# Optimization experiments

Hardware: AMD Instinct MI355X
Metric: run time of the kernel (lower is better)

## Reference

```python
import jax, jax.numpy as jnp
import numpy as np

GROUPS = 8
EPS = 1e-5
V, CIN, COUT, K, TDIM, B = 49152, 128, 256, 8, 256, 1
E = V * 9


def group_norm(x, gamma, beta):
    # x: [B, V, C]; torch GroupNorm semantics: normalize over (pixels, channels-in-group)
    b, v, c = x.shape
    xg = x.reshape(b, v, GROUPS, c // GROUPS)
    mu = xg.mean(axis=(1, 3), keepdims=True)
    var = xg.var(axis=(1, 3), keepdims=True)
    xg = (xg - mu) * jax.lax.rsqrt(var + EPS)
    return xg.reshape(b, v, c) * gamma + beta


def cheb_conv(x, row, col, vals, w):
    # x: [B, V, C]; w: [K, C, F]; Chebyshev recurrence on sparse Laplacian
    b, v, c = x.shape
    k = w.shape[0]
    xt = x.transpose(1, 0, 2).reshape(v, b * c)  # [V, B*C]

    def spmv(z):  # sparse L @ z via scatter-add
        return jnp.zeros_like(z).at[row].add(vals[:, None] * z[col])

    terms = [xt]
    if k > 1:
        terms.append(spmv(xt))
    for _ in range(k - 2):
        terms.append(2.0 * spmv(terms[-1]) - terms[-2])
    t = jnp.stack(terms).reshape(k, v, b, c)  # [K, V, B, C]
    return jnp.einsum('kvbc,kcf->bvf', t, w)  # [B, V, F]


def setup_inputs() -> dict:
    key = jax.random.key(0)
    ks = jax.random.split(key, 12)
    return {
        'x': jax.random.normal(ks[0], (B, V, CIN), jnp.float32),
        'time_emb': jax.random.normal(ks[1], (B, TDIM), jnp.float32),
        'row': jax.random.randint(ks[2], (E,), 0, V),
        'col': jax.random.randint(ks[3], (E,), 0, V),
        'vals': jax.random.normal(ks[4], (E,), jnp.float32) * 0.1,
        'w_res': jax.random.normal(ks[5], (K, CIN, COUT), jnp.float32) * 0.05,
        'w1': jax.random.normal(ks[6], (K, CIN, COUT), jnp.float32) * 0.05,
        'w2': jax.random.normal(ks[7], (K, COUT, COUT), jnp.float32) * 0.05,
        'g1': jnp.ones((CIN,), jnp.float32),
        'b1': jnp.zeros((CIN,), jnp.float32),
        'g2': jnp.ones((COUT,), jnp.float32),
        'b2': jnp.zeros((COUT,), jnp.float32),
        'wt': jax.random.normal(ks[8], (TDIM, COUT), jnp.float32) * 0.05,
        'bt': jnp.zeros((COUT,), jnp.float32),
    }


def reference(x, time_emb, row, col, vals, w_res, w1, w2, g1, b1, g2, b2, wt, bt):
    # conv_res (in_channels != out_channels), pooling = identity
    res = cheb_conv(x, row, col, vals, w_res)
    # block1: conv(silu(group_norm(x)))
    h = cheb_conv(jax.nn.silu(group_norm(x, g1, b1)), row, col, vals, w1)
    # time embedding: SiLU -> Linear -> broadcast over pixels
    h = h + (jax.nn.silu(time_emb) @ wt + bt)[:, None, :]
    # block2
    h = cheb_conv(jax.nn.silu(group_norm(h, g2, b2)), row, col, vals, w2)
    return h + res
```

## Files before the change

kernel.cpp:

```cpp
#include <hip/hip_runtime.h>
#include <cstddef>

#define V_N 49152
#define E_N 442368
#define E_PAD 589824
#define GEPS 1e-5f
#define CO 256
#define TD 256

typedef _Float16 h16;
typedef _Float16 h8v __attribute__((ext_vector_type(8)));
typedef _Float16 h4v __attribute__((ext_vector_type(4)));
typedef float f4v __attribute__((ext_vector_type(4)));

__device__ __forceinline__ void gload_lds16(const void* g, void* l) {
    __builtin_amdgcn_global_load_lds(
        (const __attribute__((address_space(1))) unsigned int*)g,
        (__attribute__((address_space(3))) unsigned int*)l, 16, 0, 0);
}

__global__ void count_edges(const int* __restrict__ row, int* __restrict__ cnt) {
    int e = blockIdx.x * blockDim.x + threadIdx.x;
    if (e < E_N) atomicAdd(&cnt[row[e]], 1);
}

__global__ void scan_rowptr(int* __restrict__ cnt, int* __restrict__ rowptr) {
    __shared__ int part[1024];
    const int CHUNK = V_N / 1024;
    int t = threadIdx.x;
    int base = t * CHUNK;
    int s = 0;
    for (int i = 0; i < CHUNK; ++i) s += (cnt[base + i] + 3) & ~3;
    part[t] = s;
    __syncthreads();
    for (int off = 1; off < 1024; off <<= 1) {
        int v = part[t];
        int add = (t >= off) ? part[t - off] : 0;
        __syncthreads();
        part[t] = v + add;
        __syncthreads();
    }
    int run = (t == 0) ? 0 : part[t - 1];
    for (int i = 0; i < CHUNK; ++i) {
        int c = cnt[base + i];
        rowptr[base + i] = run;
        cnt[base + i] = run;
        run += (c + 3) & ~3;
    }
    if (t == 1023) rowptr[V_N] = run;
}

__global__ void fill_csr(const int* __restrict__ row, const int* __restrict__ col,
                         const float* __restrict__ vals, int* __restrict__ cursor,
                         int2* __restrict__ ep) {
    int e = blockIdx.x * blockDim.x + threadIdx.x;
    if (e < E_N) {
        int r = row[e];
        int slot = atomicAdd(&cursor[r], 1);
        ep[slot] = make_int2(col[e], __float_as_int(vals[e]));
    }
}

__global__ void wprep_frag(const float* __restrict__ w, h16* __restrict__ wf) {
    int ks = blockIdx.x, nt = blockIdx.y, lane = threadIdx.x;
    int fr = lane & 15, fq = lane >> 4;
    int f = nt * 16 + fr;
    h8v o;
#pragma unroll
    for (int jj = 0; jj < 8; ++jj) {
        int kc = ks * 32 + fq * 8 + jj;
        o[jj] = (h16)w[(size_t)kc * CO + f];
    }
    *(h8v*)&wf[(((size_t)ks * 16 + nt) * 64 + lane) * 8] = o;
}

template <int C>
__global__ void gn_stats2(const float* __restrict__ x, const float* __restrict__ tvec,
                          float* __restrict__ part) {
    __shared__ float ls[8], lss[8];
    int t = threadIdx.x;
    if (t < 8) { ls[t] = 0.f; lss[t] = 0.f; }
    __syncthreads();
    const int total4 = V_N * (C / 4);
    const int cmask = (C / 4) - 1;
    const int stride = gridDim.x * blockDim.x;
    int i0 = blockIdx.x * blockDim.x + t;
    const int c4 = i0 & cmask;
    float t0 = 0.f, t1 = 0.f, t2 = 0.f, t3 = 0.f;
    if (tvec) {
        t0 = tvec[c4 * 4 + 0]; t1 = tvec[c4 * 4 + 1];
        t2 = tvec[c4 * 4 + 2]; t3 = tvec[c4 * 4 + 3];
    }
    float s = 0.f, ss = 0.f;
    for (int i = i0; i < total4; i += stride) {
        float4 v = ((const float4*)x)[i];
        v.x += t0; v.y += t1; v.z += t2; v.w += t3;
        s  += v.x + v.y + v.z + v.w;
        ss += v.x * v.x + v.y * v.y + v.z * v.z + v.w * v.w;
    }
    constexpr int GL = (C == 128) ? 4 : 8;
#pragma unroll
    for (int off = 1; off < GL; off <<= 1) {
        s  += __shfl_xor(s, off);
        ss += __shfl_xor(ss, off);
    }
    int lane = t & 63;
    if ((lane & (GL - 1)) == 0) {
        int g = c4 >> ((C == 128) ? 2 : 3);
        atomicAdd(&ls[g], s);
        atomicAdd(&lss[g], ss);
    }
    __syncthreads();
    if (t < 16) part[blockIdx.x * 16 + t] = (t < 8) ? ls[t] : lss[t - 8];
}

#define GN_BLOCKS 512

__global__ void gn_reduce(const float* __restrict__ part, float* __restrict__ stats,
                          int nb) {
    __shared__ float acc[16];
    int t = threadIdx.x;
    if (t < 16) acc[t] = 0.f;
    __syncthreads();
    int idx = t & 15;
    float s = 0.f;
    for (int j = t >> 4; j < nb; j += 16) s += part[j * 16 + idx];
    atomicAdd(&acc[idx], s);
    __syncthreads();
    if (t < 16) stats[t] = acc[t];
}

__global__ void gn1_apply(const float* __restrict__ x, const float* __restrict__ stats,
                          const float* __restrict__ gamma, const float* __restrict__ beta,
                          h16* __restrict__ dst, int ldT) {
    const float Ng = (float)V_N * 16.f;
    const int total4 = V_N * 32;
    for (int i = blockIdx.x * blockDim.x + threadIdx.x; i < total4;
         i += gridDim.x * blockDim.x) {
        int c4 = i & 31;
        int v = i >> 5;
        float4 xv = ((const float4*)x)[i];
        float in[4] = {xv.x, xv.y, xv.z, xv.w};
        h4v o, oc;
#pragma unroll
        for (int j = 0; j < 4; ++j) {
            int c = c4 * 4 + j;
            int g = c >> 4;
            float mu = stats[g] / Ng;
            float var = stats[8 + g] / Ng - mu * mu;
            float rs = rsqrtf(var + GEPS);
            float y = (in[j] - mu) * rs * gamma[c] + beta[c];
            y = y / (1.f + expf(-y));
            o[j] = (h16)y;
            oc[j] = (h16)in[j];
        }
        size_t base = (size_t)v * ldT + c4 * 4;
        *(h4v*)&dst[base] = o;
        *(h4v*)&dst[base + 128] = oc;
    }
}

__global__ void gn2_apply(const float* __restrict__ x, const float* __restrict__ tvec,
                          const float* __restrict__ stats, const float* __restrict__ gamma,
                          const float* __restrict__ beta, h16* __restrict__ dst, int ldT) {
    const float Ng = (float)V_N * 32.f;
    const int total4 = V_N * 64;
    for (int i = blockIdx.x * blockDim.x + threadIdx.x; i < total4;
         i += gridDim.x * blockDim.x) {
        int c4 = i & 63;
        int v = i >> 6;
        float4 xv = ((const float4*)x)[i];
        float in[4] = {xv.x, xv.y, xv.z, xv.w};
        h4v o;
#pragma unroll
        for (int j = 0; j < 4; ++j) {
            int c = c4 * 4 + j;
            int g = c >> 5;
            float mu = stats[g] / Ng;
            float var = stats[8 + g] / Ng - mu * mu;
            float rs = rsqrtf(var + GEPS);
            float val = in[j] + tvec[c];
            float y = (val - mu) * rs * gamma[c] + beta[c];
            y = y / (1.f + expf(-y));
            o[j] = (h16)y;
        }
        *(h4v*)&dst[(size_t)v * ldT + c4 * 4] = o;
    }
}

__global__ void time_mlp(const float* __restrict__ te, const float* __restrict__ wt,
                         const float* __restrict__ bt, float* __restrict__ tvec) {
    __shared__ float s[TD];
    int f = threadIdx.x;
    float v = te[f];
    s[f] = v / (1.f + expf(-v));
    __syncthreads();
    float acc = bt[f];
    for (int t = 0; t < TD; ++t) acc += s[t] * wt[t * CO + f];
    tvec[f] = acc;
}

template <bool RECUR>
__global__ void spmv2(const int* __restrict__ rowptr, const int2* __restrict__ ep,
                      const h16* __restrict__ zb, const h16* __restrict__ pb,
                      h16* __restrict__ db, int ldT) {
    int wid = threadIdx.x >> 6, lane = threadIdx.x & 63;
    int half = lane >> 5, hl = lane & 31;
    int v = blockIdx.x * 8 + wid * 2 + half;
    int s = rowptr[v], e = rowptr[v + 1];
    float acc[8];
#pragma unroll
    for (int i = 0; i < 8; ++i) acc[i] = 0.f;
    const int4* e4 = (const int4*)(ep + s);
    int n4 = (e - s) >> 1;
    for (int i = 0; i < n4; i += 2) {
        int4 a0 = e4[i], a1 = e4[i + 1];
        h8v z0 = *(const h8v*)&zb[(size_t)a0.x * ldT + hl * 8];
        h8v z1 = *(const h8v*)&zb[(size_t)a0.z * ldT + hl * 8];
        h8v z2 = *(const h8v*)&zb[(size_t)a1.x * ldT + hl * 8];
        h8v z3 = *(const h8v*)&zb[(size_t)a1.z * ldT + hl * 8];
        float v0 = __int_as_float(a0.y), v1 = __int_as_float(a0.w);
        float v2 = __int_as_float(a1.y), v3 = __int_as_float(a1.w);
#pragma unroll
        for (int k = 0; k < 8; ++k)
            acc[k] += v0 * (float)z0[k] + v1 * (float)z1[k] +
                      v2 * (float)z2[k] + v3 * (float)z3[k];
    }
    size_t base = (size_t)v * ldT + hl * 8;
    h8v o;
    if (RECUR) {
        h8v pv = *(const h8v*)&pb[base];
#pragma unroll
        for (int i = 0; i < 8; ++i) o[i] = (h16)(2.f * acc[i] - (float)pv[i]);
    } else {
#pragma unroll
        for (int i = 0; i < 8; ++i) o[i] = (h16)acc[i];
    }
    *(h8v*)&db[base] = o;
}

template <int MODE, bool DUAL>
__global__ __launch_bounds__(256, 3) void gemm_f16(
    const h16* __restrict__ A, int lda, const h16* __restrict__ Wf,
    const h16* __restrict__ Wf2, int wofs, int KC, int ksh,
    const float* __restrict__ bias, float* __restrict__ out,
    float* __restrict__ out2) {
    __shared__ h16 As[2][128 * 32];
    if (DUAL && blockIdx.y) { A += 128; Wf = Wf2; out = out2; }
    const int bid = blockIdx.x;
    const int xcd = bid & 7;
    const int j = bid >> 3;
    const int mblk = xcd * 48 + (j >> 1);
    const int nh = j & 1;
    const int m0 = mblk * 128;
    const int n0 = nh * 128;
    const int tid = threadIdx.x;
    const int wid = tid >> 6, lane = tid & 63;
    const int wm = wid & 1, wn = wid >> 1;
    const int fr = lane & 15, fq = lane >> 4;
    const int rl = lane >> 2;
    const int qs = (lane & 3) ^ ((lane >> 3) & 3);
    const int kmsk = (1 << ksh) - 1;
    const h16* Arow0 = A + (size_t)(m0 + wid * 16 + rl) * lda;
    const h16* Arow1 = A + (size_t)(m0 + (wid + 4) * 16 + rl) * lda;
    const h16* Wlane = Wf + ((size_t)(wofs >> 5) * 16 * 512) + (size_t)lane * 8;
    const int ntb = (n0 >> 4) + wn * 4;

    f4v acc[4][4];
#pragma unroll
    for (int i = 0; i < 4; ++i)
#pragma unroll
        for (int n = 0; n < 4; ++n) acc[i][n] = (f4v){0.f, 0.f, 0.f, 0.f};

    const int nt = KC >> 5;
    auto stageA = [&](int t, int buf) {
        int kk = t << 5;
        int ca = (((kk >> ksh) << 8) | (kk & kmsk)) + qs * 8;
        gload_lds16(Arow0 + ca, &As[buf][(wid * 16) * 32]);
        gload_lds16(Arow1 + ca, &As[buf][((wid + 4) * 16) * 32]);
    };
    h8v bfc[4], bfn[4];
    stageA(0, 0);
#pragma unroll
    for (int n = 0; n < 4; ++n)
        bfc[n] = *(const h8v*)&Wlane[(size_t)(ntb + n) * 512];
    __syncthreads();

    const int slot = (fq ^ ((fr >> 1) & 3)) * 8;
    for (int t = 0; t < nt; ++t) {
        const int cur = t & 1;
        h8v af[4];
#pragma unroll
        for (int i = 0; i < 4; ++i)
            af[i] = *(const h8v*)&As[cur][(wm * 64 + i * 16 + fr) * 32 + slot];
        int tn = (t + 1 < nt) ? t + 1 : t;
        stageA(tn, cur ^ 1);
#pragma unroll
        for (int n = 0; n < 4; ++n)
            bfn[n] = *(const h8v*)&Wlane[((size_t)tn * 16 + ntb + n) * 512];
#pragma unroll
        for (int i = 0; i < 4; ++i)
#pragma unroll
            for (int n = 0; n < 4; ++n)
                acc[i][n] = __builtin_amdgcn_mfma_f32_16x16x32_f16(af[i], bfc[n],
                                                                   acc[i][n], 0, 0, 0);
        __syncthreads();
#pragma unroll
        for (int n = 0; n < 4; ++n) bfc[n] = bfn[n];
    }
#pragma unroll
    for (int i = 0; i < 4; ++i)
#pragma unroll
        for (int n = 0; n < 4; ++n)
#pragma unroll
            for (int rr = 0; rr < 4; ++rr) {
                int row = m0 + wm * 64 + i * 16 + fq * 4 + rr;
                int col = n0 + wn * 64 + n * 16 + fr;
                size_t idx = (size_t)row * CO + col;
                if (MODE == 0) out[idx] = acc[i][n][rr];
                else if (MODE == 1) out[idx] += acc[i][n][rr];
                else out[idx] = bias[idx] + acc[i][n][rr];
            }
}

static void chain_spmv(hipStream_t s, int chunk, int k0, int kend, h16* terms, int ldT,
                       const int* rp, const int2* ep) {
    for (int k = (k0 == 0 ? 1 : k0); k < kend; ++k) {
        const h16* zb = terms + ((k - 1) % chunk) * 256;
        h16* db = terms + (k % chunk) * 256;
        if (k == 1) {
            spmv2<false><<<V_N / 8, 256, 0, s>>>(rp, ep, zb, nullptr, db, ldT);
        } else {
            const h16* pb = terms + ((k - 2) % chunk) * 256;
            spmv2<true><<<V_N / 8, 256, 0, s>>>(rp, ep, zb, pb, db, ldT);
        }
    }
}

extern "C" void kernel_launch(void* const* d_in, const int* in_sizes, int n_in,
                              void* d_out, int out_size, void* d_ws, size_t ws_size,
                              hipStream_t stream) {
    const float* x    = (const float*)d_in[0];
    const float* te   = (const float*)d_in[1];
    const int*   row  = (const int*)d_in[2];
    const int*   col  = (const int*)d_in[3];
    const float* vals = (const float*)d_in[4];
    const float* wres = (const float*)d_in[5];
    const float* w1   = (const float*)d_in[6];
    const float* w2   = (const float*)d_in[7];
    const float* g1   = (const float*)d_in[8];
    const float* b1   = (const float*)d_in[9];
    const float* g2   = (const float*)d_in[10];
    const float* b2   = (const float*)d_in[11];
    const float* wt   = (const float*)d_in[12];
    const float* bt   = (const float*)d_in[13];
    float* out = (float*)d_out;

    const size_t slot_b = (size_t)V_N * 256 * 2;
    const size_t res_b  = (size_t)V_N * 256 * 4;
    const size_t csr_b  = (size_t)(V_N + V_N + 1) * 4 + (size_t)E_PAD * 8;
    const size_t wt_b   = (size_t)(1024 + 2048 + 1024) * CO * 2;
    const size_t misc_b = 8192 + (size_t)GN_BLOCKS * 16 * 4;
    auto need = [&](int ch) { return (size_t)ch * slot_b + res_b + csr_b + wt_b + misc_b; };
    int chunk = (ws_size >= need(8)) ? 8 : (ws_size >= need(4)) ? 4 : 2;
    if (ws_size < need(2)) return;
    const int ldT = chunk * 256;

    char* p = (char*)d_ws;
    h16* terms = (h16*)p;              p += (size_t)chunk * slot_b;
    float* resbuf = (float*)p;         p += res_b;
    h16* w1f = (h16*)p;                p += (size_t)1024 * CO * 2;
    h16* w2f = (h16*)p;                p += (size_t)2048 * CO * 2;
    h16* wrf = (h16*)p;                p += (size_t)1024 * CO * 2;
    int* cnt = (int*)p;                p += (size_t)V_N * 4;
    int* rp  = (int*)p;                p += (size_t)(V_N + 1) * 4;
    int2* ep = (int2*)p;               p += (size_t)E_PAD * 8;
    float* stats = (float*)p;          p += 64;
    float* tv = (float*)p;             p += 1024;
    float* gpart = (float*)p;          p += (size_t)GN_BLOCKS * 16 * 4;

    hipMemsetAsync(cnt, 0, V_N * sizeof(int), stream);
    hipMemsetAsync(ep, 0, (size_t)E_PAD * 8, stream);
    count_edges<<<E_N / 256, 256, 0, stream>>>(row, cnt);
    scan_rowptr<<<1, 1024, 0, stream>>>(cnt, rp);
    fill_csr<<<E_N / 256, 256, 0, stream>>>(row, col, vals, cnt, ep);

    wprep_frag<<<dim3(32, 16), 64, 0, stream>>>(w1, w1f);
    wprep_frag<<<dim3(64, 16), 64, 0, stream>>>(w2, w2f);
    wprep_frag<<<dim3(32, 16), 64, 0, stream>>>(wres, wrf);

    time_mlp<<<1, 256, 0, stream>>>(te, wt, bt, tv);

    gn_stats2<128><<<GN_BLOCKS, 256, 0, stream>>>(x, nullptr, gpart);
    gn_reduce<<<1, 256, 0, stream>>>(gpart, stats, GN_BLOCKS);
    gn1_apply<<<2048, 256, 0, stream>>>(x, stats, g1, b1, terms, ldT);

    for (int k0 = 0; k0 < 8; k0 += chunk) {
        int kend = (k0 + chunk < 8) ? k0 + chunk : 8;
        chain_spmv(stream, chunk, k0, kend, terms, ldT, rp, ep);
        int KC = (kend - k0) * 128;
        dim3 g(V_N / 128 * 2, 2);
        if (k0 == 0)
            gemm_f16<0, true><<<g, 256, 0, stream>>>(terms, ldT, w1f, wrf,
                                                     k0 * 128, KC, 7, nullptr, out, resbuf);
        else
            gemm_f16<1, true><<<g, 256, 0, stream>>>(terms, ldT, w1f, wrf,
                                                     k0 * 128, KC, 7, nullptr, out, resbuf);
    }

    gn_stats2<256><<<GN_BLOCKS, 256, 0, stream>>>(out, tv, gpart);
    gn_reduce<<<1, 256, 0, stream>>>(gpart, stats, GN_BLOCKS);
    gn2_apply<<<2048, 256, 0, stream>>>(out, tv, stats, g2, b2, terms, ldT);

    for (int k0 = 0; k0 < 8; k0 += chunk) {
        int kend = (k0 + chunk < 8) ? k0 + chunk : 8;
        chain_spmv(stream, chunk, k0, kend, terms, ldT, rp, ep);
        int KC = (kend - k0) * 256;
        dim3 g(V_N / 128 * 2);
        if (k0 == 0)
            gemm_f16<2, false><<<g, 256, 0, stream>>>(terms, ldT, w2f, nullptr,
                                                      0, KC, 8, resbuf, out, nullptr);
        else
            gemm_f16<1, false><<<g, 256, 0, stream>>>(terms, ldT, w2f, nullptr,
                                                      k0 * 256, KC, 8, nullptr, out, nullptr);
    }
}
```

Before: 841.1 us.

## Store Chebyshev terms in channel-sliced swizzled layout for SpMV locality

Changes the term buffer from a row-major [V, chunk*256] layout to per-slice [slice][V][32] half-precision blocks with an XOR swizzle. SpMV is split across 8 channel slices per node group, so each gather reads a compact 64-byte row inside a smaller working set that fits cache better. The GEMM A-staging reads contiguous 128x32 tiles directly, and the chunk is fixed at 8, dropping the smaller-workspace fallback. The cost is that each slice's SpMV rereads the CSR edge list, giving 8x more edge-index traffic.

Result: faster. 796.7 us, median of 2 (-5.3%).

```diff
diff --git a/kernel.cpp b/kernel.cpp
--- a/kernel.cpp
+++ b/kernel.cpp
@@ -10,8 +10,8 @@
 
 typedef _Float16 h16;
 typedef _Float16 h8v __attribute__((ext_vector_type(8)));
-typedef _Float16 h4v __attribute__((ext_vector_type(4)));
 typedef float f4v __attribute__((ext_vector_type(4)));
+
 
 __device__ __forceinline__ void gload_lds16(const void* g, void* l) {
     __builtin_amdgcn_global_load_lds(
@@ -132,19 +132,19 @@
 
 __global__ void gn1_apply(const float* __restrict__ x, const float* __restrict__ stats,
                           const float* __restrict__ gamma, const float* __restrict__ beta,
-                          h16* __restrict__ dst, int ldT) {
+                          h16* __restrict__ terms) {
     const float Ng = (float)V_N * 16.f;
-    const int total4 = V_N * 32;
-    for (int i = blockIdx.x * blockDim.x + threadIdx.x; i < total4;
+    const int total = V_N * 16;
+    for (int i = blockIdx.x * blockDim.x + threadIdx.x; i < total;
          i += gridDim.x * blockDim.x) {
-        int c4 = i & 31;
-        int v = i >> 5;
-        float4 xv = ((const float4*)x)[i];
-        float in[4] = {xv.x, xv.y, xv.z, xv.w};
-        h4v o, oc;
-#pragma unroll
-        for (int j = 0; j < 4; ++j) {
-            int c = c4 * 4 + j;
+        int v = i >> 4, c8 = i & 15;
+        float4 xa = ((const float4*)x)[v * 32 + c8 * 2];
+        float4 xb = ((const float4*)x)[v * 32 + c8 * 2 + 1];
+        float in[8] = {xa.x, xa.y, xa.z, xa.w, xb.x, xb.y, xb.z, xb.w};
+        h8v o, oc;
+#pragma unroll
+        for (int j = 0; j < 8; ++j) {
+            int c = c8 * 8 + j;
             int g = c >> 4;
             float mu = stats[g] / Ng;
             float var = stats[8 + g] / Ng - mu * mu;
@@ -154,27 +154,28 @@
             o[j] = (h16)y;
             oc[j] = (h16)in[j];
         }
-        size_t base = (size_t)v * ldT + c4 * 4;
-        *(h4v*)&dst[base] = o;
-        *(h4v*)&dst[base + 128] = oc;
+        int qsl = ((c8 & 3) ^ ((v >> 1) & 3)) * 8;
+        int slice = c8 >> 2;
+        *(h8v*)&terms[((size_t)slice * V_N + v) * 32 + qsl] = o;
+        *(h8v*)&terms[((size_t)(4 + slice) * V_N + v) * 32 + qsl] = oc;
     }
 }
 
 __global__ void gn2_apply(const float* __restrict__ x, const float* __restrict__ tvec,
                           const float* __restrict__ stats, const float* __restrict__ gamma,
-                          const float* __restrict__ beta, h16* __restrict__ dst, int ldT) {
+                          const float* __restrict__ beta, h16* __restrict__ terms) {
     const float Ng = (float)V_N * 32.f;
-    const int total4 = V_N * 64;
-    for (int i = blockIdx.x * blockDim.x + threadIdx.x; i < total4;
+    const int total = V_N * 32;
+    for (int i = blockIdx.x * blockDim.x + threadIdx.x; i < total;
          i += gridDim.x * blockDim.x) {
-        int c4 = i & 63;
-        int v = i >> 6;
-        float4 xv = ((const float4*)x)[i];
-        float in[4] = {xv.x, xv.y, xv.z, xv.w};
-        h4v o;
-#pragma unroll
-        for (int j = 0; j < 4; ++j) {
-            int c = c4 * 4 + j;
+        int v = i >> 5, c8 = i & 31;
+        float4 xa = ((const float4*)x)[v * 64 + c8 * 2];
+        float4 xb = ((const float4*)x)[v * 64 + c8 * 2 + 1];
+        float in[8] = {xa.x, xa.y, xa.z, xa.w, xb.x, xb.y, xb.z, xb.w};
+        h8v o;
+#pragma unroll
+        for (int j = 0; j < 8; ++j) {
+            int c = c8 * 8 + j;
             int g = c >> 5;
             float mu = stats[g] / Ng;
             float var = stats[8 + g] / Ng - mu * mu;
@@ -184,7 +185,9 @@
             y = y / (1.f + expf(-y));
             o[j] = (h16)y;
         }
-        *(h4v*)&dst[(size_t)v * ldT + c4 * 4] = o;
+        int qsl = ((c8 & 3) ^ ((v >> 1) & 3)) * 8;
+        int slice = c8 >> 2;
+        *(h8v*)&terms[((size_t)slice * V_N + v) * 32 + qsl] = o;
     }
 }
 
@@ -201,12 +204,14 @@
 }
 
 template <bool RECUR>
-__global__ void spmv2(const int* __restrict__ rowptr, const int2* __restrict__ ep,
-                      const h16* __restrict__ zb, const h16* __restrict__ pb,
-                      h16* __restrict__ db, int ldT) {
-    int wid = threadIdx.x >> 6, lane = threadIdx.x & 63;
-    int half = lane >> 5, hl = lane & 31;
-    int v = blockIdx.x * 8 + wid * 2 + half;
+__global__ void spmv_slice(const int* __restrict__ rowptr, const int2* __restrict__ ep,
+                           h16* __restrict__ terms, int zs, int ps, int ds) {
+    const int slice = blockIdx.x & 7;
+    const int wid = threadIdx.x >> 6, lane = threadIdx.x & 63;
+    const int eg = lane >> 2, q = lane & 3;
+    const int v = (blockIdx.x >> 3) * 64 + wid * 16 + eg;
+    const h16* zb = terms + ((size_t)(zs * 8 + slice) * V_N) * 32;
+    h16* db = terms + ((size_t)(ds * 8 + slice) * V_N) * 32;
     int s = rowptr[v], e = rowptr[v + 1];
     float acc[8];
 #pragma unroll
@@ -215,10 +220,10 @@
     int n4 = (e - s) >> 1;
     for (int i = 0; i < n4; i += 2) {
         int4 a0 = e4[i], a1 = e4[i + 1];
-        h8v z0 = *(const h8v*)&zb[(size_t)a0.x * ldT + hl * 8];
-        h8v z1 = *(const h8v*)&zb[(size_t)a0.z * ldT + hl * 8];
-        h8v z2 = *(const h8v*)&zb[(size_t)a1.x * ldT + hl * 8];
-        h8v z3 = *(const h8v*)&zb[(size_t)a1.z * ldT + hl * 8];
+        h8v z0 = *(const h8v*)&zb[(size_t)a0.x * 32 + ((q ^ ((a0.x >> 1) & 3)) * 8)];
+        h8v z1 = *(const h8v*)&zb[(size_t)a0.z * 32 + ((q ^ ((a0.z >> 1) & 3)) * 8)];
+        h8v z2 = *(const h8v*)&zb[(size_t)a1.x * 32 + ((q ^ ((a1.x >> 1) & 3)) * 8)];
+        h8v z3 = *(const h8v*)&zb[(size_t)a1.z * 32 + ((q ^ ((a1.z >> 1) & 3)) * 8)];
         float v0 = __int_as_float(a0.y), v1 = __int_as_float(a0.w);
         float v2 = __int_as_float(a1.y), v3 = __int_as_float(a1.w);
 #pragma unroll
@@ -226,9 +231,10 @@
             acc[k] += v0 * (float)z0[k] + v1 * (float)z1[k] +
                       v2 * (float)z2[k] + v3 * (float)z3[k];
     }
-    size_t base = (size_t)v * ldT + hl * 8;
+    size_t base = (size_t)v * 32 + ((q ^ ((v >> 1) & 3)) * 8);
     h8v o;
     if (RECUR) {
+        const h16* pb = terms + ((size_t)(ps * 8 + slice) * V_N) * 32;
         h8v pv = *(const h8v*)&pb[base];
 #pragma unroll
         for (int i = 0; i < 8; ++i) o[i] = (h16)(2.f * acc[i] - (float)pv[i]);
@@ -241,12 +247,13 @@
 
 template <int MODE, bool DUAL>
 __global__ __launch_bounds__(256, 3) void gemm_f16(
-    const h16* __restrict__ A, int lda, const h16* __restrict__ Wf,
-    const h16* __restrict__ Wf2, int wofs, int KC, int ksh,
+    const h16* __restrict__ terms, const h16* __restrict__ Wf,
+    const h16* __restrict__ Wf2, int kslot0, int wofs, int KC, int slsh,
     const float* __restrict__ bias, float* __restrict__ out,
     float* __restrict__ out2) {
     __shared__ h16 As[2][128 * 32];
-    if (DUAL && blockIdx.y) { A += 128; Wf = Wf2; out = out2; }
+    int sofs = 0;
+    if (DUAL && blockIdx.y) { Wf = Wf2; out = out2; sofs = 4; }
     const int bid = blockIdx.x;
     const int xcd = bid & 7;
     const int j = bid >> 3;
@@ -258,11 +265,7 @@
     const int wid = tid >> 6, lane = tid & 63;
     const int wm = wid & 1, wn = wid >> 1;
     const int fr = lane & 15, fq = lane >> 4;
-    const int rl = lane >> 2;
-    const int qs = (lane & 3) ^ ((lane >> 3) & 3);
-    const int kmsk = (1 << ksh) - 1;
-    const h16* Arow0 = A + (size_t)(m0 + wid * 16 + rl) * lda;
-    const h16* Arow1 = A + (size_t)(m0 + (wid + 4) * 16 + rl) * lda;
+    const int smsk = (1 << slsh) - 1;
     const h16* Wlane = Wf + ((size_t)(wofs >> 5) * 16 * 512) + (size_t)lane * 8;
     const int ntb = (n0 >> 4) + wn * 4;
 
@@ -274,10 +277,11 @@
 
     const int nt = KC >> 5;
     auto stageA = [&](int t, int buf) {
-        int kk = t << 5;
-        int ca = (((kk >> ksh) << 8) | (kk & kmsk)) + qs * 8;
-        gload_lds16(Arow0 + ca, &As[buf][(wid * 16) * 32]);
-        gload_lds16(Arow1 + ca, &As[buf][((wid + 4) * 16) * 32]);
+        int r8 = (kslot0 + (t >> slsh)) * 8 + ((t & smsk) + sofs);
+        const h16* b = terms + ((size_t)r8 * V_N + m0) * 32;
+        gload_lds16(b + (size_t)(wid * 16) * 32 + lane * 8, &As[buf][(wid * 16) * 32]);
+        gload_lds16(b + (size_t)((wid + 4) * 16) * 32 + lane * 8,
+                    &As[buf][((wid + 4) * 16) * 32]);
     };
     h8v bfc[4], bfn[4];
     stageA(0, 0);
@@ -323,16 +327,15 @@
             }
 }
 
-static void chain_spmv(hipStream_t s, int chunk, int k0, int kend, h16* terms, int ldT,
+static void chain_spmv(hipStream_t s, int chunk, int k0, int kend, h16* terms,
                        const int* rp, const int2* ep) {
     for (int k = (k0 == 0 ? 1 : k0); k < kend; ++k) {
-        const h16* zb = terms + ((k - 1) % chunk) * 256;
-        h16* db = terms + (k % chunk) * 256;
+        int zs = (k - 1) % chunk, ds = k % chunk;
         if (k == 1) {
-            spmv2<false><<<V_N / 8, 256, 0, s>>>(rp, ep, zb, nullptr, db, ldT);
+            spmv_slice<false><<<V_N / 64 * 8, 256, 0, s>>>(rp, ep, terms, zs, 0, ds);
         } else {
-            const h16* pb = terms + ((k - 2) % chunk) * 256;
-            spmv2<true><<<V_N / 8, 256, 0, s>>>(rp, ep, zb, pb, db, ldT);
+            int ps = (k - 2) % chunk;
+            spmv_slice<true><<<V_N / 64 * 8, 256, 0, s>>>(rp, ep, terms, zs, ps, ds);
         }
     }
 }
@@ -356,15 +359,13 @@
     const float* bt   = (const float*)d_in[13];
     float* out = (float*)d_out;
 
+    const int chunk = 8;
     const size_t slot_b = (size_t)V_N * 256 * 2;
     const size_t res_b  = (size_t)V_N * 256 * 4;
     const size_t csr_b  = (size_t)(V_N + V_N + 1) * 4 + (size_t)E_PAD * 8;
     const size_t wt_b   = (size_t)(1024 + 2048 + 1024) * CO * 2;
     const size_t misc_b = 8192 + (size_t)GN_BLOCKS * 16 * 4;
-    auto need = [&](int ch) { return (size_t)ch * slot_b + res_b + csr_b + wt_b + misc_b; };
-    int chunk = (ws_size >= need(8)) ? 8 : (ws_size >= need(4)) ? 4 : 2;
-    if (ws_size < need(2)) return;
-    const int ldT = chunk * 256;
+    if (ws_size < (size_t)chunk * slot_b + res_b + csr_b + wt_b + misc_b) return;
 
     char* p = (char*)d_ws;
     h16* terms = (h16*)p;              p += (size_t)chunk * slot_b;
@@ -393,35 +394,23 @@
 
     gn_stats2<128><<<GN_BLOCKS, 256, 0, stream>>>(x, nullptr, gpart);
     gn_reduce<<<1, 256, 0, stream>>>(gpart, stats, GN_BLOCKS);
-    gn1_apply<<<2048, 256, 0, stream>>>(x, stats, g1, b1, terms, ldT);
-
-    for (int k0 = 0; k0 < 8; k0 += chunk) {
-        int kend = (k0 + chunk < 8) ? k0 + chunk : 8;
-        chain_spmv(stream, chunk, k0, kend, terms, ldT, rp, ep);
-        int KC = (kend - k0) * 128;
+    gn1_apply<<<3072, 256, 0, stream>>>(x, stats, g1, b1, terms);
+
+    chain_spmv(stream, chunk, 0, 8, terms, rp, ep);
+    {
         dim3 g(V_N / 128 * 2, 2);
-        if (k0 == 0)
-            gemm_f16<0, true><<<g, 256, 0, stream>>>(terms, ldT, w1f, wrf,
-                                                     k0 * 128, KC, 7, nullptr, out, resbuf);
-        else
-            gemm_f16<1, true><<<g, 256, 0, stream>>>(terms, ldT, w1f, wrf,
-                                                     k0 * 128, KC, 7, nullptr, out, resbuf);
+        gemm_f16<0, true><<<g, 256, 0, stream>>>(terms, w1f, wrf, 0, 0, 1024, 2,
+                                                 nullptr, out, resbuf);
     }
 
     gn_stats2<256><<<GN_BLOCKS, 256, 0, stream>>>(out, tv, gpart);
     gn_reduce<<<1, 256, 0, stream>>>(gpart, stats, GN_BLOCKS);
-    gn2_apply<<<2048, 256, 0, stream>>>(out, tv, stats, g2, b2, terms, ldT);
-
-    for (int k0 = 0; k0 < 8; k0 += chunk) {
-        int kend = (k0 + chunk < 8) ? k0 + chunk : 8;
-        chain_spmv(stream, chunk, k0, kend, terms, ldT, rp, ep);
-        int KC = (kend - k0) * 256;
+    gn2_apply<<<6144, 256, 0, stream>>>(out, tv, stats, g2, b2, terms);
+
+    chain_spmv(stream, chunk, 0, 8, terms, rp, ep);
+    {
         dim3 g(V_N / 128 * 2);
-        if (k0 == 0)
-            gemm_f16<2, false><<<g, 256, 0, stream>>>(terms, ldT, w2f, nullptr,
-                                                      0, KC, 8, resbuf, out, nullptr);
-        else
-            gemm_f16<1, false><<<g, 256, 0, stream>>>(terms, ldT, w2f, nullptr,
-                                                      k0 * 256, KC, 8, nullptr, out, nullptr);
-    }
-}
+        gemm_f16<2, false><<<g, 256, 0, stream>>>(terms, w2f, nullptr, 0, 0, 2048, 3,
+                                                  resbuf, out, nullptr);
+    }
+}
```
